# Kernel optimization log

Measured on AMD Instinct MI355X. Metric: run time of the kernel, lower is better.

The kernel has to match this reference:

```python
import jax, jax.numpy as jnp
import numpy as np

BATCH, SEQ, D_MODEL, STATE_DIM = 16, 4096, 512, 512


def _xavier(key, shape):
    fan_in, fan_out = shape[1], shape[0]
    limit = float(np.sqrt(6.0 / (fan_in + fan_out)))
    return jax.random.uniform(key, shape, jnp.float32, -limit, limit)


def setup_inputs() -> dict:
    key = jax.random.key(0)
    kx, ka, kb, kc = jax.random.split(key, 4)
    x = jax.random.normal(kx, (BATCH, SEQ, D_MODEL), jnp.float32)
    A = _xavier(ka, (STATE_DIM, STATE_DIM))
    B = _xavier(kb, (STATE_DIM, D_MODEL))
    C = _xavier(kc, (D_MODEL, STATE_DIM))
    return {"x": x, "A": A, "B": B, "C": C}


def reference(x, A, B, C):
    # x: [batch, seq, d_model]; state: [batch, state_dim]
    batch = x.shape[0]
    state0 = jnp.zeros((batch, A.shape[0]), x.dtype)

    # Precompute input projection for all timesteps: [seq, batch, state_dim]
    bx = jnp.einsum('btd,nd->tbn', x, B)

    def step(state, bx_t):
        # state_{t} = relu(state_{t-1} @ A^T + B @ x_t)
        state = jax.nn.relu(state @ A.T + bx_t)
        y = state @ C.T  # [batch, d_model]
        return state, y

    _, ys = jax.lax.scan(step, state0, bx)
    return jnp.transpose(ys, (1, 0, 2))  # [batch, seq, d_model]
```

## Files before the change

kernel.cpp:

```cpp
#include <hip/hip_runtime.h>
#include <hip/hip_bf16.h>

typedef __attribute__((ext_vector_type(4))) float  fvec4;
typedef __attribute__((ext_vector_type(8))) short  svec8;
typedef __attribute__((ext_vector_type(8))) unsigned short usvec8;
typedef __attribute__((ext_vector_type(4))) unsigned short usvec4;
typedef __attribute__((ext_vector_type(2))) unsigned int   uivec2;
typedef __attribute__((ext_vector_type(4))) unsigned int   uivec4;

#define MFMA16 __builtin_amdgcn_mfma_f32_16x16x32_bf16

static __device__ __forceinline__ unsigned short f2bf(float f) {
    __hip_bfloat16 h = __float2bfloat16(f);
    return __builtin_bit_cast(unsigned short, h);
}
static __device__ __forceinline__ float bf2f(unsigned short u) {
    unsigned int v = ((unsigned int)u) << 16;
    return __builtin_bit_cast(float, v);
}

__global__ void cvt_kernel(const float* __restrict__ in, unsigned short* __restrict__ out, int n4) {
    int stride = gridDim.x * blockDim.x;
    for (int i = blockIdx.x * blockDim.x + threadIdx.x; i < n4; i += stride) {
        fvec4 v = ((const fvec4*)in)[i];
        usvec4 u;
        u[0] = f2bf(v[0]); u[1] = f2bf(v[1]); u[2] = f2bf(v[2]); u[3] = f2bf(v[3]);
        ((usvec4*)out)[i] = u;
    }
}

template<bool LHS_F32_PERM, bool OUT_PERM>
__global__ __launch_bounds__(256)
void gemm512(const void* __restrict__ lhsv, const unsigned short* __restrict__ rhs,
             void* __restrict__ outv)
{
    __shared__ __align__(16) unsigned short smA[64 * 72];
    __shared__ __align__(16) unsigned short smB[64 * 72];
    const int tid = threadIdx.x;
    const int m0 = blockIdx.x * 64;
    const int n0 = blockIdx.y * 64;
    const int w = tid >> 6, l = tid & 63;
    const int g = l >> 4, r16 = l & 15;
    const int wm = (w >> 1) * 32, wn = (w & 1) * 32;
    const int ri = tid >> 2;
    const int kseg = (tid & 3) * 16;

    fvec4 acc[2][2] = {};

    for (int k0 = 0; k0 < 512; k0 += 64) {
        if (LHS_F32_PERM) {
            const float* x = (const float*)lhsv;
            int m = m0 + ri;
            size_t base = ((size_t)(m & 15) * 4096 + (size_t)(m >> 4)) * 512 + k0 + kseg;
            usvec8 o0, o1;
            fvec4 v0 = *(const fvec4*)(x + base + 0);
            fvec4 v1 = *(const fvec4*)(x + base + 4);
            fvec4 v2 = *(const fvec4*)(x + base + 8);
            fvec4 v3 = *(const fvec4*)(x + base + 12);
            o0[0]=f2bf(v0[0]); o0[1]=f2bf(v0[1]); o0[2]=f2bf(v0[2]); o0[3]=f2bf(v0[3]);
            o0[4]=f2bf(v1[0]); o0[5]=f2bf(v1[1]); o0[6]=f2bf(v1[2]); o0[7]=f2bf(v1[3]);
            o1[0]=f2bf(v2[0]); o1[1]=f2bf(v2[1]); o1[2]=f2bf(v2[2]); o1[3]=f2bf(v2[3]);
            o1[4]=f2bf(v3[0]); o1[5]=f2bf(v3[1]); o1[6]=f2bf(v3[2]); o1[7]=f2bf(v3[3]);
            *(usvec8*)(smA + ri * 72 + kseg)     = o0;
            *(usvec8*)(smA + ri * 72 + kseg + 8) = o1;
        } else {
            const unsigned short* s = (const unsigned short*)lhsv;
            size_t base = (size_t)(m0 + ri) * 512 + k0 + kseg;
            *(usvec8*)(smA + ri * 72 + kseg)     = *(const usvec8*)(s + base);
            *(usvec8*)(smA + ri * 72 + kseg + 8) = *(const usvec8*)(s + base + 8);
        }
        {
            size_t base = (size_t)(n0 + ri) * 512 + k0 + kseg;
            *(usvec8*)(smB + ri * 72 + kseg)     = *(const usvec8*)(rhs + base);
            *(usvec8*)(smB + ri * 72 + kseg + 8) = *(const usvec8*)(rhs + base + 8);
        }
        __syncthreads();
        #pragma unroll
        for (int kt = 0; kt < 2; ++kt) {
            svec8 a0 = *(const svec8*)(smA + (wm +      r16) * 72 + 32 * kt + 8 * g);
            svec8 a1 = *(const svec8*)(smA + (wm + 16 + r16) * 72 + 32 * kt + 8 * g);
            svec8 b0 = *(const svec8*)(smB + (wn +      r16) * 72 + 32 * kt + 8 * g);
            svec8 b1 = *(const svec8*)(smB + (wn + 16 + r16) * 72 + 32 * kt + 8 * g);
            acc[0][0] = MFMA16(a0, b0, acc[0][0], 0, 0, 0);
            acc[0][1] = MFMA16(a0, b1, acc[0][1], 0, 0, 0);
            acc[1][0] = MFMA16(a1, b0, acc[1][0], 0, 0, 0);
            acc[1][1] = MFMA16(a1, b1, acc[1][1], 0, 0, 0);
        }
        __syncthreads();
    }
    #pragma unroll
    for (int mt = 0; mt < 2; ++mt)
    #pragma unroll
    for (int nt = 0; nt < 2; ++nt)
    #pragma unroll
    for (int r = 0; r < 4; ++r) {
        int m = m0 + wm + 16 * mt + 4 * g + r;
        int n = n0 + wn + 16 * nt + r16;
        float v = acc[mt][nt][r];
        if (OUT_PERM) {
            float* out = (float*)outv;
            out[((size_t)(m & 15) * 4096 + (size_t)(m >> 4)) * 512 + n] = v;
        } else {
            unsigned short* out = (unsigned short*)outv;
            out[(size_t)m * 512 + n] = f2bf(v);
        }
    }
}

#define RT 4096

#define LDSB(KT) (*(const svec8*)(stp + ((64 * (KT) + 16 * g) ^ swz)))
#define LDSA(J, KT) (*(const svec8*)(ldsA + (((w * 2 + (J)) * 16 + (KT)) << 9) + l * 8))

#define MFA(ACC, AF, SB) asm("v_mfma_f32_16x16x32_bf16 %0, %1, %2, %0" : "+v"(ACC) : "a"(AF), "v"(SB))
#define MFV(ACC, AF, SB) asm("v_mfma_f32_16x16x32_bf16 %0, %1, %2, %0" : "+v"(ACC) : "v"(AF), "v"(SB))

#define KTSTEP(KT) do { \
    sbv[((KT) + 2) % 3] = LDSB((KT) + 2); \
    s6a[((KT) + 2) % 3] = LDSA(0, (KT) + 2); \
    s7a[((KT) + 2) % 3] = LDSA(1, (KT) + 2); \
    svec8 sc = sbv[(KT) % 3]; \
    MFA(acc[0], af_a[KT][0], sc); \
    MFA(acc[1], af_a[KT][1], sc); \
    MFA(acc[2], af_a[KT][2], sc); \
    MFA(acc[3], af_a[KT][3], sc); \
    MFV(acc[4], af_v[KT][0], sc); \
    MFV(acc[5], af_v[KT][1], sc); \
    MFV(acc[6], s6a[(KT) % 3], sc); \
    MFV(acc[7], s7a[(KT) % 3], sc); \
    __builtin_amdgcn_sched_barrier(0); \
} while (0)

#define KTSTEPNP(KT) do { \
    svec8 sc = sbv[(KT) % 3]; \
    MFA(acc[0], af_a[KT][0], sc); \
    MFA(acc[1], af_a[KT][1], sc); \
    MFA(acc[2], af_a[KT][2], sc); \
    MFA(acc[3], af_a[KT][3], sc); \
    MFV(acc[4], af_v[KT][0], sc); \
    MFV(acc[5], af_v[KT][1], sc); \
    MFV(acc[6], s6a[(KT) % 3], sc); \
    MFV(acc[7], s7a[(KT) % 3], sc); \
    __builtin_amdgcn_sched_barrier(0); \
} while (0)

__global__ __launch_bounds__(256, 1)
void recur1cu_kernel(const unsigned short* __restrict__ Abf,
                     const unsigned short* __restrict__ bx,
                     unsigned short* __restrict__ states)
{
    __shared__ __align__(16) unsigned short st[2][16 * 512];
    __shared__ __align__(16) unsigned short ldsA[4 * 2 * 16 * 512];
    const int tid = threadIdx.x;
    const int w = tid >> 6, l = tid & 63;
    const int g = l >> 4, r16 = l & 15;
    const int nbase = w * 128;
    const int swz = (r16 & 7) << 4;

    #pragma unroll
    for (int j = 0; j < 2; ++j)
        #pragma unroll
        for (int kt = 0; kt < 16; ++kt) {
            usvec8 v = *(const usvec8*)(Abf + (size_t)(nbase + 16 * (6 + j) + r16) * 512
                                        + 32 * kt + 8 * g);
            *(usvec8*)(ldsA + (((w * 2 + j) * 16 + kt) << 9) + l * 8) = v;
        }

    svec8 af_a[16][4];
    #pragma unroll
    for (int kt = 0; kt < 16; ++kt)
        #pragma unroll
        for (int mt = 0; mt < 4; ++mt)
            af_a[kt][mt] = *(const svec8*)(Abf + (size_t)(nbase + 16 * mt + r16) * 512
                                           + 32 * kt + 8 * g);

    svec8 af_v[16][2];
    #pragma unroll
    for (int kt = 0; kt < 16; ++kt)
        #pragma unroll
        for (int j = 0; j < 2; ++j)
            af_v[kt][j] = *(const svec8*)(Abf + (size_t)(nbase + 16 * (4 + j) + r16) * 512
                                          + 32 * kt + 8 * g);

    {
        const unsigned short* bp = bx + (size_t)r16 * 512 + nbase + 4 * g;
        char* stq = (char*)&st[0][0] + r16 * 1024;
        #pragma unroll
        for (int mt = 0; mt < 8; ++mt) {
            unsigned long long u = *(const unsigned long long*)(bp + 16 * mt);
            float f0 = fmaxf(bf2f((unsigned short)( u        & 0xffffu)), 0.0f);
            float f1 = fmaxf(bf2f((unsigned short)((u >> 16) & 0xffffu)), 0.0f);
            float f2 = fmaxf(bf2f((unsigned short)((u >> 32) & 0xffffu)), 0.0f);
            float f3 = fmaxf(bf2f((unsigned short)((u >> 48) & 0xffffu)), 0.0f);
            unsigned int plo, phi;
            asm("v_cvt_pk_bf16_f32 %0, %1, %2" : "=v"(plo) : "v"(f0), "v"(f1));
            asm("v_cvt_pk_bf16_f32 %0, %1, %2" : "=v"(phi) : "v"(f2), "v"(f3));
            uivec2 ov; ov[0] = plo; ov[1] = phi;
            *(uivec2*)(stq + ((2 * (nbase + 16 * mt + 4 * g)) ^ swz)) = ov;
        }
    }
    __syncthreads();

    const int erow = 4 * w + (l >> 4);
    const int eswz = (erow & 7) << 4;
    const int ecol = (l & 15) * 16;

    #pragma unroll 1
    for (int t = 1; t < RT; ++t) {
        const char* stbase_p = (const char*)&st[(t - 1) & 1][0];

        {
            const char* sp = stbase_p + erow * 1024;
            char* gp = (char*)states + ((size_t)(t - 1) * 16 + erow) * 1024 + ecol;
            #pragma unroll
            for (int jj = 0; jj < 4; ++jj) {
                uivec4 v = *(const uivec4*)(sp + ((ecol + 256 * jj) ^ eswz));
                *(uivec4*)(gp + 256 * jj) = v;
            }
        }

        unsigned long long bq[8];
        {
            const unsigned short* bp = bx + ((size_t)t * 16 + r16) * 512 + nbase + 4 * g;
            #pragma unroll
            for (int mt = 0; mt < 8; ++mt)
                bq[mt] = *(const unsigned long long*)(bp + 16 * mt);
        }

        fvec4 acc[8];
        #pragma unroll
        for (int mt = 0; mt < 8; ++mt) acc[mt] = fvec4{0.f, 0.f, 0.f, 0.f};
        asm volatile("s_nop 1"
                     : "+v"(acc[0]), "+v"(acc[1]), "+v"(acc[2]), "+v"(acc[3]),
                       "+v"(acc[4]), "+v"(acc[5]), "+v"(acc[6]), "+v"(acc[7]));

        const char* stp = stbase_p + r16 * 1024;
        svec8 sbv[3], s6a[3], s7a[3];
        sbv[0] = LDSB(0); sbv[1] = LDSB(1);
        s6a[0] = LDSA(0, 0); s6a[1] = LDSA(0, 1);
        s7a[0] = LDSA(1, 0); s7a[1] = LDSA(1, 1);
        KTSTEP(0);  KTSTEP(1);  KTSTEP(2);  KTSTEP(3);
        KTSTEP(4);  KTSTEP(5);  KTSTEP(6);  KTSTEP(7);
        KTSTEP(8);  KTSTEP(9);  KTSTEP(10); KTSTEP(11);
        KTSTEP(12); KTSTEP(13); KTSTEPNP(14); KTSTEPNP(15);

        asm volatile("s_nop 7\n\ts_nop 7"
                     : "+v"(acc[0]), "+v"(acc[1]), "+v"(acc[2]), "+v"(acc[3]),
                       "+v"(acc[4]), "+v"(acc[5]), "+v"(acc[6]), "+v"(acc[7]));

        {
            char* stq = (char*)&st[t & 1][0] + r16 * 1024;
            #pragma unroll
            for (int mt = 0; mt < 8; ++mt) {
                unsigned long long u = bq[mt];
                float f0 = fmaxf(acc[mt][0] + bf2f((unsigned short)( u        & 0xffffu)), 0.0f);
                float f1 = fmaxf(acc[mt][1] + bf2f((unsigned short)((u >> 16) & 0xffffu)), 0.0f);
                float f2 = fmaxf(acc[mt][2] + bf2f((unsigned short)((u >> 32) & 0xffffu)), 0.0f);
                float f3 = fmaxf(acc[mt][3] + bf2f((unsigned short)((u >> 48) & 0xffffu)), 0.0f);
                unsigned int plo, phi;
                asm("v_cvt_pk_bf16_f32 %0, %1, %2" : "=v"(plo) : "v"(f0), "v"(f1));
                asm("v_cvt_pk_bf16_f32 %0, %1, %2" : "=v"(phi) : "v"(f2), "v"(f3));
                uivec2 ov; ov[0] = plo; ov[1] = phi;
                *(uivec2*)(stq + ((2 * (nbase + 16 * mt + 4 * g)) ^ swz)) = ov;
            }
        }

        __syncthreads();
    }

    {
        const char* sp = (const char*)&st[(RT - 1) & 1][0] + erow * 1024;
        char* gp = (char*)states + ((size_t)(RT - 1) * 16 + erow) * 1024 + ecol;
        #pragma unroll
        for (int jj = 0; jj < 4; ++jj) {
            uivec4 v = *(const uivec4*)(sp + ((ecol + 256 * jj) ^ eswz));
            *(uivec4*)(gp + 256 * jj) = v;
        }
    }
}

extern "C" void kernel_launch(void* const* d_in, const int* in_sizes, int n_in,
                              void* d_out, int out_size, void* d_ws, size_t ws_size,
                              hipStream_t stream) {
    const float* x = (const float*)d_in[0];
    const float* A = (const float*)d_in[1];
    const float* B = (const float*)d_in[2];
    const float* C = (const float*)d_in[3];
    float* out = (float*)d_out;

    char* ws = (char*)d_ws;
    unsigned short* Abf = (unsigned short*)(ws + 0);
    unsigned short* Bbf = (unsigned short*)(ws + (size_t)(1 << 19));
    unsigned short* Cbf = (unsigned short*)(ws + (size_t)(2 << 19));
    unsigned short* bx  = (unsigned short*)(ws + (size_t)(4 << 19));
    unsigned short* states = (unsigned short*)(ws + (size_t)(4 << 19) + ((size_t)1 << 26));

    cvt_kernel<<<64, 256, 0, stream>>>(A, Abf, 512 * 512 / 4);
    cvt_kernel<<<64, 256, 0, stream>>>(B, Bbf, 512 * 512 / 4);
    cvt_kernel<<<64, 256, 0, stream>>>(C, Cbf, 512 * 512 / 4);

    dim3 grid(1024, 8);
    gemm512<true, false><<<grid, 256, 0, stream>>>((const void*)x, Bbf, (void*)bx);
    recur1cu_kernel<<<1, 256, 0, stream>>>(Abf, bx, states);
    gemm512<false, true><<<grid, 256, 0, stream>>>((const void*)states, Cbf, (void*)out);
}
```

Before: 7.499 ms.

## Pipeline own-slice state MFMAs of the next step before the barrier

Each wave's K-chunk order is rotated so its last four chunks are the state columns that wave itself produces. Right after the ReLU/bf16 epilogue writes those columns, the wave starts the next timestep's MFMAs on them, interleaved with the remaining epilogue work and before the block-wide barrier. After the barrier only the other twelve chunks remain, which shortens the serial per-step critical path. The costs are a more intricate schedule, a prologue that seeds step one's partial sums, and reliance on same-wave LDS write-then-read ordering.

```diff
diff --git a/kernel.cpp b/kernel.cpp
--- a/kernel.cpp
+++ b/kernel.cpp
@@ -109,39 +109,56 @@
 
 #define RT 4096
 
-#define LDSB(KT) (*(const svec8*)(stp + ((64 * (KT) + 16 * g) ^ swz)))
-#define LDSA(J, KT) (*(const svec8*)(ldsA + (((w * 2 + (J)) * 16 + (KT)) << 9) + l * 8))
-
-#define MFA(ACC, AF, SB) asm("v_mfma_f32_16x16x32_bf16 %0, %1, %2, %0" : "+v"(ACC) : "a"(AF), "v"(SB))
-#define MFV(ACC, AF, SB) asm("v_mfma_f32_16x16x32_bf16 %0, %1, %2, %0" : "+v"(ACC) : "v"(AF), "v"(SB))
-
-#define KTSTEP(KT) do { \
-    sbv[((KT) + 2) % 3] = LDSB((KT) + 2); \
-    s6a[((KT) + 2) % 3] = LDSA(0, (KT) + 2); \
-    s7a[((KT) + 2) % 3] = LDSA(1, (KT) + 2); \
-    svec8 sc = sbv[(KT) % 3]; \
-    MFA(acc[0], af_a[KT][0], sc); \
-    MFA(acc[1], af_a[KT][1], sc); \
-    MFA(acc[2], af_a[KT][2], sc); \
-    MFA(acc[3], af_a[KT][3], sc); \
-    MFV(acc[4], af_v[KT][0], sc); \
-    MFV(acc[5], af_v[KT][1], sc); \
-    MFV(acc[6], s6a[(KT) % 3], sc); \
-    MFV(acc[7], s7a[(KT) % 3], sc); \
-    __builtin_amdgcn_sched_barrier(0); \
+#define LDSBP(I) (*(const svec8*)(stp + ((kb[I] + 16 * g) ^ swz)))
+#define LDSBQ(P, I) (*(const svec8*)((P) + ((kb[I] + 16 * g) ^ swz)))
+#define LDSA(J, I) (*(const svec8*)(ldsA + (((w * 2 + (J)) * 16 + (I)) << 9) + l * 8))
+
+#define MFA(ACC, AF, SB)  asm("v_mfma_f32_16x16x32_bf16 %0, %1, %2, %0" : "+v"(ACC) : "a"(AF), "v"(SB))
+#define MFV(ACC, AF, SB)  asm("v_mfma_f32_16x16x32_bf16 %0, %1, %2, %0" : "+v"(ACC) : "v"(AF), "v"(SB))
+#define MFA0(ACC, AF, SB) asm("v_mfma_f32_16x16x32_bf16 %0, %1, %2, 0"  : "=v"(ACC) : "a"(AF), "v"(SB))
+#define MFV0(ACC, AF, SB) asm("v_mfma_f32_16x16x32_bf16 %0, %1, %2, 0"  : "=v"(ACC) : "v"(AF), "v"(SB))
+#define SBAR __builtin_amdgcn_sched_barrier(0)
+
+#define FSTEP(I) do { \
+    sbv[((I) + 2) % 3] = LDSBP((I) + 2); \
+    s6a[((I) + 2) % 3] = LDSA(0, (I) + 2); \
+    s7a[((I) + 2) % 3] = LDSA(1, (I) + 2); \
+    svec8 sc = sbv[(I) % 3]; \
+    MFA(acc[0], af_a[I][0], sc); \
+    MFA(acc[1], af_a[I][1], sc); \
+    MFA(acc[2], af_a[I][2], sc); \
+    MFA(acc[3], af_a[I][3], sc); \
+    MFV(acc[4], af_v[I][0], sc); \
+    MFV(acc[5], af_v[I][1], sc); \
+    MFV(acc[6], s6a[(I) % 3], sc); \
+    MFV(acc[7], s7a[(I) % 3], sc); \
+    SBAR; \
 } while (0)
 
-#define KTSTEPNP(KT) do { \
-    svec8 sc = sbv[(KT) % 3]; \
-    MFA(acc[0], af_a[KT][0], sc); \
-    MFA(acc[1], af_a[KT][1], sc); \
-    MFA(acc[2], af_a[KT][2], sc); \
-    MFA(acc[3], af_a[KT][3], sc); \
-    MFV(acc[4], af_v[KT][0], sc); \
-    MFV(acc[5], af_v[KT][1], sc); \
-    MFV(acc[6], s6a[(KT) % 3], sc); \
-    MFV(acc[7], s7a[(KT) % 3], sc); \
-    __builtin_amdgcn_sched_barrier(0); \
+#define FSTEPNP(I) do { \
+    svec8 sc = sbv[(I) % 3]; \
+    MFA(acc[0], af_a[I][0], sc); \
+    MFA(acc[1], af_a[I][1], sc); \
+    MFA(acc[2], af_a[I][2], sc); \
+    MFA(acc[3], af_a[I][3], sc); \
+    MFV(acc[4], af_v[I][0], sc); \
+    MFV(acc[5], af_v[I][1], sc); \
+    MFV(acc[6], s6a[(I) % 3], sc); \
+    MFV(acc[7], s7a[(I) % 3], sc); \
+    SBAR; \
+} while (0)
+
+#define EP(MT) do { \
+    unsigned long long _u = bq[MT]; \
+    float _f0 = fmaxf(acc[MT][0] + bf2f((unsigned short)( _u        & 0xffffu)), 0.0f); \
+    float _f1 = fmaxf(acc[MT][1] + bf2f((unsigned short)((_u >> 16) & 0xffffu)), 0.0f); \
+    float _f2 = fmaxf(acc[MT][2] + bf2f((unsigned short)((_u >> 32) & 0xffffu)), 0.0f); \
+    float _f3 = fmaxf(acc[MT][3] + bf2f((unsigned short)((_u >> 48) & 0xffffu)), 0.0f); \
+    unsigned int _plo, _phi; \
+    asm("v_cvt_pk_bf16_f32 %0, %1, %2" : "=v"(_plo) : "v"(_f0), "v"(_f1)); \
+    asm("v_cvt_pk_bf16_f32 %0, %1, %2" : "=v"(_phi) : "v"(_f2), "v"(_f3)); \
+    uivec2 _ov; _ov[0] = _plo; _ov[1] = _phi; \
+    *(uivec2*)(stq + ((2 * (nbase + 16 * (MT) + 4 * g)) ^ swz)) = _ov; \
 } while (0)
 
 __global__ __launch_bounds__(256, 1)
@@ -157,34 +174,37 @@
     const int nbase = w * 128;
     const int swz = (r16 & 7) << 4;
 
+    int kp[16], kb[16];
+    #pragma unroll
+    for (int i = 0; i < 16; ++i) { kp[i] = (4 * w + 4 + i) & 15; kb[i] = kp[i] * 64; }
+
     #pragma unroll
     for (int j = 0; j < 2; ++j)
         #pragma unroll
-        for (int kt = 0; kt < 16; ++kt) {
+        for (int i = 0; i < 16; ++i) {
             usvec8 v = *(const usvec8*)(Abf + (size_t)(nbase + 16 * (6 + j) + r16) * 512
-                                        + 32 * kt + 8 * g);
-            *(usvec8*)(ldsA + (((w * 2 + j) * 16 + kt) << 9) + l * 8) = v;
+                                        + 32 * kp[i] + 8 * g);
+            *(usvec8*)(ldsA + (((w * 2 + j) * 16 + i) << 9) + l * 8) = v;
         }
 
     svec8 af_a[16][4];
     #pragma unroll
-    for (int kt = 0; kt < 16; ++kt)
+    for (int i = 0; i < 16; ++i)
         #pragma unroll
         for (int mt = 0; mt < 4; ++mt)
-            af_a[kt][mt] = *(const svec8*)(Abf + (size_t)(nbase + 16 * mt + r16) * 512
-                                           + 32 * kt + 8 * g);
-
+            af_a[i][mt] = *(const svec8*)(Abf + (size_t)(nbase + 16 * mt + r16) * 512
+                                          + 32 * kp[i] + 8 * g);
     svec8 af_v[16][2];
     #pragma unroll
-    for (int kt = 0; kt < 16; ++kt)
+    for (int i = 0; i < 16; ++i)
         #pragma unroll
         for (int j = 0; j < 2; ++j)
-            af_v[kt][j] = *(const svec8*)(Abf + (size_t)(nbase + 16 * (4 + j) + r16) * 512
-                                          + 32 * kt + 8 * g);
+            af_v[i][j] = *(const svec8*)(Abf + (size_t)(nbase + 16 * (4 + j) + r16) * 512
+                                         + 32 * kp[i] + 8 * g);
 
     {
         const unsigned short* bp = bx + (size_t)r16 * 512 + nbase + 4 * g;
-        char* stq = (char*)&st[0][0] + r16 * 1024;
+        char* st0 = (char*)&st[0][0] + r16 * 1024;
         #pragma unroll
         for (int mt = 0; mt < 8; ++mt) {
             unsigned long long u = *(const unsigned long long*)(bp + 16 * mt);
@@ -196,8 +216,34 @@
             asm("v_cvt_pk_bf16_f32 %0, %1, %2" : "=v"(plo) : "v"(f0), "v"(f1));
             asm("v_cvt_pk_bf16_f32 %0, %1, %2" : "=v"(phi) : "v"(f2), "v"(f3));
             uivec2 ov; ov[0] = plo; ov[1] = phi;
-            *(uivec2*)(stq + ((2 * (nbase + 16 * mt + 4 * g)) ^ swz)) = ov;
-        }
+            *(uivec2*)(st0 + ((2 * (nbase + 16 * mt + 4 * g)) ^ swz)) = ov;
+        }
+    }
+
+    fvec4 acc[8];
+
+    {
+        const char* sq = (const char*)&st[0][0] + r16 * 1024;
+        svec8 sb12 = LDSBQ(sq, 12), sb13 = LDSBQ(sq, 13);
+        svec8 sb14 = LDSBQ(sq, 14), sb15 = LDSBQ(sq, 15);
+        svec8 t6a = LDSA(0, 12), t6b = LDSA(0, 13), t6c = LDSA(0, 14), t6d = LDSA(0, 15);
+        svec8 t7a = LDSA(1, 12), t7b = LDSA(1, 13), t7c = LDSA(1, 14), t7d = LDSA(1, 15);
+        MFA0(acc[0], af_a[12][0], sb12);  MFA0(acc[1], af_a[12][1], sb12);
+        MFA0(acc[2], af_a[12][2], sb12);  MFA0(acc[3], af_a[12][3], sb12);
+        MFV0(acc[4], af_v[12][0], sb12);  MFV0(acc[5], af_v[12][1], sb12);
+        MFV0(acc[6], t6a, sb12);          MFV0(acc[7], t7a, sb12);
+        MFA(acc[0], af_a[13][0], sb13);   MFA(acc[1], af_a[13][1], sb13);
+        MFA(acc[2], af_a[13][2], sb13);   MFA(acc[3], af_a[13][3], sb13);
+        MFV(acc[4], af_v[13][0], sb13);   MFV(acc[5], af_v[13][1], sb13);
+        MFV(acc[6], t6b, sb13);           MFV(acc[7], t7b, sb13);
+        MFA(acc[0], af_a[14][0], sb14);   MFA(acc[1], af_a[14][1], sb14);
+        MFA(acc[2], af_a[14][2], sb14);   MFA(acc[3], af_a[14][3], sb14);
+        MFV(acc[4], af_v[14][0], sb14);   MFV(acc[5], af_v[14][1], sb14);
+        MFV(acc[6], t6c, sb14);           MFV(acc[7], t7c, sb14);
+        MFA(acc[0], af_a[15][0], sb15);   MFA(acc[1], af_a[15][1], sb15);
+        MFA(acc[2], af_a[15][2], sb15);   MFA(acc[3], af_a[15][3], sb15);
+        MFV(acc[4], af_v[15][0], sb15);   MFV(acc[5], af_v[15][1], sb15);
+        MFV(acc[6], t6d, sb15);           MFV(acc[7], t7d, sb15);
     }
     __syncthreads();
 
@@ -208,6 +254,7 @@
     #pragma unroll 1
     for (int t = 1; t < RT; ++t) {
         const char* stbase_p = (const char*)&st[(t - 1) & 1][0];
+        char* stq = (char*)&st[t & 1][0] + r16 * 1024;
 
         {
             const char* sp = stbase_p + erow * 1024;
@@ -227,43 +274,65 @@
                 bq[mt] = *(const unsigned long long*)(bp + 16 * mt);
         }
 
-        fvec4 acc[8];
-        #pragma unroll
-        for (int mt = 0; mt < 8; ++mt) acc[mt] = fvec4{0.f, 0.f, 0.f, 0.f};
-        asm volatile("s_nop 1"
-                     : "+v"(acc[0]), "+v"(acc[1]), "+v"(acc[2]), "+v"(acc[3]),
-                       "+v"(acc[4]), "+v"(acc[5]), "+v"(acc[6]), "+v"(acc[7]));
-
         const char* stp = stbase_p + r16 * 1024;
         svec8 sbv[3], s6a[3], s7a[3];
-        sbv[0] = LDSB(0); sbv[1] = LDSB(1);
+        sbv[0] = LDSBP(0); sbv[1] = LDSBP(1);
         s6a[0] = LDSA(0, 0); s6a[1] = LDSA(0, 1);
         s7a[0] = LDSA(1, 0); s7a[1] = LDSA(1, 1);
-        KTSTEP(0);  KTSTEP(1);  KTSTEP(2);  KTSTEP(3);
-        KTSTEP(4);  KTSTEP(5);  KTSTEP(6);  KTSTEP(7);
-        KTSTEP(8);  KTSTEP(9);  KTSTEP(10); KTSTEP(11);
-        KTSTEP(12); KTSTEP(13); KTSTEPNP(14); KTSTEPNP(15);
+        FSTEP(0); FSTEP(1); FSTEP(2); FSTEP(3); FSTEP(4);
+        FSTEP(5); FSTEP(6); FSTEP(7); FSTEP(8); FSTEP(9);
+        FSTEPNP(10); FSTEPNP(11);
 
         asm volatile("s_nop 7\n\ts_nop 7"
                      : "+v"(acc[0]), "+v"(acc[1]), "+v"(acc[2]), "+v"(acc[3]),
                        "+v"(acc[4]), "+v"(acc[5]), "+v"(acc[6]), "+v"(acc[7]));
 
-        {
-            char* stq = (char*)&st[t & 1][0] + r16 * 1024;
-            #pragma unroll
-            for (int mt = 0; mt < 8; ++mt) {
-                unsigned long long u = bq[mt];
-                float f0 = fmaxf(acc[mt][0] + bf2f((unsigned short)( u        & 0xffffu)), 0.0f);
-                float f1 = fmaxf(acc[mt][1] + bf2f((unsigned short)((u >> 16) & 0xffffu)), 0.0f);
-                float f2 = fmaxf(acc[mt][2] + bf2f((unsigned short)((u >> 32) & 0xffffu)), 0.0f);
-                float f3 = fmaxf(acc[mt][3] + bf2f((unsigned short)((u >> 48) & 0xffffu)), 0.0f);
-                unsigned int plo, phi;
-                asm("v_cvt_pk_bf16_f32 %0, %1, %2" : "=v"(plo) : "v"(f0), "v"(f1));
-                asm("v_cvt_pk_bf16_f32 %0, %1, %2" : "=v"(phi) : "v"(f2), "v"(f3));
-                uivec2 ov; ov[0] = plo; ov[1] = phi;
-                *(uivec2*)(stq + ((2 * (nbase + 16 * mt + 4 * g)) ^ swz)) = ov;
-            }
-        }
+        EP(0); EP(1);
+        svec8 sb12 = LDSBQ(stq, 12);
+        MFA0(acc[0], af_a[12][0], sb12);
+        MFA0(acc[1], af_a[12][1], sb12);
+        SBAR;
+        EP(2); EP(3);
+        svec8 sb13 = LDSBQ(stq, 13);
+        MFA0(acc[2], af_a[12][2], sb12);
+        MFA0(acc[3], af_a[12][3], sb12);
+        MFA(acc[0], af_a[13][0], sb13);
+        MFA(acc[1], af_a[13][1], sb13);
+        MFA(acc[2], af_a[13][2], sb13);
+        MFA(acc[3], af_a[13][3], sb13);
+        SBAR;
+        EP(4); EP(5);
+        svec8 sb14 = LDSBQ(stq, 14);
+        MFV0(acc[4], af_v[12][0], sb12);
+        MFV0(acc[5], af_v[12][1], sb12);
+        MFV(acc[4], af_v[13][0], sb13);
+        MFV(acc[5], af_v[13][1], sb13);
+        MFA(acc[0], af_a[14][0], sb14);
+        MFA(acc[1], af_a[14][1], sb14);
+        MFA(acc[2], af_a[14][2], sb14);
+        MFA(acc[3], af_a[14][3], sb14);
+        SBAR;
+        EP(6); EP(7);
+        svec8 sb15 = LDSBQ(stq, 15);
+        svec8 t6a = LDSA(0, 12), t6b = LDSA(0, 13), t6c = LDSA(0, 14), t6d = LDSA(0, 15);
+        svec8 t7a = LDSA(1, 12), t7b = LDSA(1, 13), t7c = LDSA(1, 14), t7d = LDSA(1, 15);
+        MFA(acc[0], af_a[15][0], sb15);
+        MFA(acc[1], af_a[15][1], sb15);
+        MFA(acc[2], af_a[15][2], sb15);
+        MFA(acc[3], af_a[15][3], sb15);
+        MFV(acc[4], af_v[14][0], sb14);
+        MFV(acc[5], af_v[14][1], sb14);
+        MFV(acc[4], af_v[15][0], sb15);
+        MFV(acc[5], af_v[15][1], sb15);
+        MFV0(acc[6], t6a, sb12);
+        MFV0(acc[7], t7a, sb12);
+        MFV(acc[6], t6b, sb13);
+        MFV(acc[7], t7b, sb13);
+        MFV(acc[6], t6c, sb14);
+        MFV(acc[7], t7c, sb14);
+        MFV(acc[6], t6d, sb15);
+        MFV(acc[7], t7d, sb15);
+        SBAR;
 
         __syncthreads();
     }
```

New measurement: 7.450 ms. About the same (-0.6%).
